# Optimization experiments

Hardware: AMD Instinct MI355X
Metric: run time of the kernel (lower is better)

Reference implementation:

```python
import jax, jax.numpy as jnp
import numpy as np

N_NODES, IN_DIM, HEADS, HEAD_DIM, OUT_DIM, N_GRAPHS, N_EDGES = 100000, 3, 4, 16, 2, 512, 3200000
NEG_SLOPE = 0.2  # PyG GATConv default negative_slope


def setup_inputs() -> dict:
    key = jax.random.key(0)
    ks = jax.random.split(key, 8)
    HC = HEADS * HEAD_DIM
    x = jax.random.normal(ks[0], (N_NODES, IN_DIM), dtype=jnp.float32)
    edge_index = jax.random.randint(ks[1], (2, N_EDGES), 0, N_NODES, dtype=jnp.int64)
    # sorted graph ids covering all N_GRAPHS segments (avoids empty-segment -inf in max pool)
    batch = (jnp.arange(N_NODES, dtype=jnp.int64) * N_GRAPHS) // N_NODES
    glorot = lambda k, shape, fan: jax.random.normal(k, shape, dtype=jnp.float32) * (1.0 / np.sqrt(fan))
    W = glorot(ks[2], (IN_DIM, HC), IN_DIM)          # GATConv lin weight
    att_src = glorot(ks[3], (HEADS, HEAD_DIM), HEAD_DIM)
    att_dst = glorot(ks[4], (HEADS, HEAD_DIM), HEAD_DIM)
    bias = jnp.zeros((HC,), dtype=jnp.float32)       # GATConv bias (concat=True)
    clf_W = glorot(ks[5], (HC, OUT_DIM), HC)
    clf_b = jnp.zeros((OUT_DIM,), dtype=jnp.float32)
    return {"feature_matrix": x, "edge_index": edge_index, "batch": batch,
            "W": W, "att_src": att_src, "att_dst": att_dst, "bias": bias,
            "clf_W": clf_W, "clf_b": clf_b}


def _gat_forward(x, edge_index, batch, W, att_src, att_dst, bias, clf_W, clf_b):
    N = x.shape[0]
    # PyG GATConv default: add self loops
    ar = jnp.arange(N, dtype=edge_index.dtype)
    ei = jnp.concatenate([edge_index, jnp.stack([ar, ar])], axis=1)
    src, dst = ei[0], ei[1]
    h = (x @ W).reshape(N, HEADS, HEAD_DIM)                     # [N,H,C]
    a_src = jnp.einsum('nhc,hc->nh', h, att_src)                # [N,H]
    a_dst = jnp.einsum('nhc,hc->nh', h, att_dst)
    e = jax.nn.leaky_relu(a_src[src] + a_dst[dst], NEG_SLOPE)   # [E,H]
    # softmax over edges grouped by destination node (every node has a self loop)
    m = jax.ops.segment_max(e, dst, num_segments=N)
    p = jnp.exp(e - m[dst])
    s = jax.ops.segment_sum(p, dst, num_segments=N)
    alpha = p / s[dst]                                          # [E,H]
    msg = h[src] * alpha[:, :, None]                            # [E,H,C]
    out = jax.ops.segment_sum(msg, dst, num_segments=N).reshape(N, HEADS * HEAD_DIM) + bias
    out = jax.nn.relu(out)
    pooled = jax.ops.segment_max(out, batch, num_segments=N_GRAPHS)  # [G,HC]
    return pooled @ clf_W + clf_b                               # [G,OUT]


def reference(feature_matrix, edge_index, batch, W, att_src, att_dst, bias, clf_W, clf_b):
    return _gat_forward(feature_matrix, edge_index, batch, W, att_src, att_dst, bias, clf_W, clf_b)
```

## Files before the change

### kernel.cpp

```cpp
#include <hip/hip_runtime.h>

#define NN 100000
#define NE 3200000
#define NE4 (NE / 4)
#define NG 512
#define OUTD 2
#define NEG_SLOPE 0.2f

#define CAP 81
#define BSZ 98
#define NSTR 1021
#define SCAP 3712
#define ADLS 5
#define EDGE_BLOCKS 256

__global__ __launch_bounds__(1024) void bin_kernel(const int* __restrict__ ei,
                                                   int* __restrict__ gcnt,
                                                   int* __restrict__ stream_) {
    __shared__ int cnt[NSTR];
    __shared__ int off[NSTR];
    int eb = blockIdx.x;
    int start = eb * 3125;
    int end = min(start + 3125, NE4);
    for (int i = threadIdx.x; i < NSTR; i += 1024) cnt[i] = 0;
    __syncthreads();
    int4 sv[4], dv[4];
    #pragma unroll
    for (int k = 0; k < 4; ++k) {
        int i4 = start + k * 1024 + threadIdx.x;
        if (i4 < end) {
            sv[k] = ((const int4*)ei)[i4];
            dv[k] = ((const int4*)(ei + NE))[i4];
            atomicAdd(&cnt[dv[k].x / BSZ], 1);
            atomicAdd(&cnt[dv[k].y / BSZ], 1);
            atomicAdd(&cnt[dv[k].z / BSZ], 1);
            atomicAdd(&cnt[dv[k].w / BSZ], 1);
        }
    }
    __syncthreads();
    for (int i = threadIdx.x; i < NSTR; i += 1024)
        off[i] = cnt[i] ? atomicAdd(&gcnt[i], cnt[i]) : 0;
    __syncthreads();
    #pragma unroll
    for (int k = 0; k < 4; ++k) {
        int i4 = start + k * 1024 + threadIdx.x;
        if (i4 < end) {
            int b, l, p;
            b = dv[k].x / BSZ; l = dv[k].x - b * BSZ; p = atomicAdd(&off[b], 1);
            stream_[(size_t)b * SCAP + p] = sv[k].x | (l << 17);
            b = dv[k].y / BSZ; l = dv[k].y - b * BSZ; p = atomicAdd(&off[b], 1);
            stream_[(size_t)b * SCAP + p] = sv[k].y | (l << 17);
            b = dv[k].z / BSZ; l = dv[k].z - b * BSZ; p = atomicAdd(&off[b], 1);
            stream_[(size_t)b * SCAP + p] = sv[k].z | (l << 17);
            b = dv[k].w / BSZ; l = dv[k].w - b * BSZ; p = atomicAdd(&off[b], 1);
            stream_[(size_t)b * SCAP + p] = sv[k].w | (l << 17);
        }
    }
}

__global__ __launch_bounds__(512) void gather_kernel(
        const int* __restrict__ gcnt, const int* __restrict__ stream_,
        const float* __restrict__ x, const float* __restrict__ W,
        const float* __restrict__ att_src, const float* __restrict__ att_dst,
        const float* __restrict__ bias, const int* __restrict__ batch,
        unsigned* __restrict__ pooled) {
    __shared__ int slots[BSZ * CAP];
    __shared__ int scnt[BSZ];
    __shared__ float xl[BSZ * 3];
    __shared__ float adl[BSZ * ADLS];
    __shared__ float Wl[192];
    __shared__ float wsS[12], wdS[12];
    __shared__ unsigned ploc[2 * 64];
    int b = blockIdx.x;
    int nbase = b * BSZ;
    if (nbase >= NN) return;
    int nloc = min(BSZ, NN - nbase);
    int tid = threadIdx.x;

    for (int i = tid; i < 192; i += 512) Wl[i] = W[i];
    for (int i = tid; i < nloc * 3; i += 512) xl[i] = x[nbase * 3 + i];
    if (tid < 24) {
        int t = tid % 12, j = t >> 2, h = t & 3;
        const float* att = (tid < 12) ? att_src : att_dst;
        float s = 0.f;
        #pragma unroll
        for (int c = 0; c < 16; ++c) s += W[j * 64 + h * 16 + c] * att[h * 16 + c];
        if (tid < 12) wsS[t] = s; else wdS[t] = s;
    }
    for (int i = tid; i < BSZ; i += 512) scnt[i] = 0;
    for (int i = tid; i < 128; i += 512) ploc[i] = 0;
    __syncthreads();
    for (int i = tid; i < nloc * 4; i += 512) {
        int l = i >> 2, h = i & 3;
        adl[l * ADLS + h] = xl[l * 3] * wdS[h] + xl[l * 3 + 1] * wdS[4 + h]
                          + xl[l * 3 + 2] * wdS[8 + h];
    }
    __syncthreads();

    int eg = gcnt[b];
    const int* st = stream_ + (size_t)b * SCAP;
    for (int i = tid; i < eg; i += 512) {
        int v = st[i];
        int s = v & 0x1FFFF;
        int l = v >> 17;
        int p = atomicAdd(&scnt[l], 1);
        if (p < CAP) slots[l * CAP + p] = s;
    }
    __syncthreads();

    int gbase = batch[nbase];
    int g = tid >> 2, head = tid & 3;
    if (g < nloc) {
        int n = nbase + g;
        float ws0 = wsS[head], ws1 = wsS[4 + head], ws2 = wsS[8 + head];
        float adh = adl[g * ADLS + head];
        float lx0 = xl[g * 3], lx1 = xl[g * 3 + 1], lx2 = xl[g * 3 + 2];

        float e = lx0 * ws0 + lx1 * ws1 + lx2 * ws2 + adh;
        e = e > 0.f ? e : NEG_SLOPE * e;
        float p = __expf(e);
        float sh = p, sx0 = p * lx0, sx1 = p * lx1, sx2 = p * lx2;

        int d = min(scnt[g], CAP);
        const int* row = &slots[g * CAP];
        int j = 0;
        for (; j + 3 < d; j += 4) {
            int sA = row[j], sB = row[j + 1], sC = row[j + 2], sD = row[j + 3];
            float xA0 = x[sA * 3], xA1 = x[sA * 3 + 1], xA2 = x[sA * 3 + 2];
            float xB0 = x[sB * 3], xB1 = x[sB * 3 + 1], xB2 = x[sB * 3 + 2];
            float xC0 = x[sC * 3], xC1 = x[sC * 3 + 1], xC2 = x[sC * 3 + 2];
            float xD0 = x[sD * 3], xD1 = x[sD * 3 + 1], xD2 = x[sD * 3 + 2];
            float eA = xA0 * ws0 + xA1 * ws1 + xA2 * ws2 + adh; eA = eA > 0.f ? eA : NEG_SLOPE * eA;
            float eB = xB0 * ws0 + xB1 * ws1 + xB2 * ws2 + adh; eB = eB > 0.f ? eB : NEG_SLOPE * eB;
            float eC = xC0 * ws0 + xC1 * ws1 + xC2 * ws2 + adh; eC = eC > 0.f ? eC : NEG_SLOPE * eC;
            float eD = xD0 * ws0 + xD1 * ws1 + xD2 * ws2 + adh; eD = eD > 0.f ? eD : NEG_SLOPE * eD;
            float pA = __expf(eA), pB = __expf(eB), pC = __expf(eC), pD = __expf(eD);
            sh  += (pA + pB) + (pC + pD);
            sx0 += pA * xA0 + pB * xB0 + pC * xC0 + pD * xD0;
            sx1 += pA * xA1 + pB * xB1 + pC * xC1 + pD * xD1;
            sx2 += pA * xA2 + pB * xB2 + pC * xC2 + pD * xD2;
        }
        for (; j < d; ++j) {
            int sA = row[j];
            float xA0 = x[sA * 3], xA1 = x[sA * 3 + 1], xA2 = x[sA * 3 + 2];
            float eA = xA0 * ws0 + xA1 * ws1 + xA2 * ws2 + adh; eA = eA > 0.f ? eA : NEG_SLOPE * eA;
            float pA = __expf(eA);
            sh += pA; sx0 += pA * xA0; sx1 += pA * xA1; sx2 += pA * xA2;
        }

        float inv = 1.f / sh;
        sx0 *= inv; sx1 *= inv; sx2 *= inv;
        int gl = batch[n] - gbase;
        unsigned* pb = ploc + gl * 64 + head * 16;
        const float* w0 = Wl + head * 16;
        const float* w1 = Wl + 64 + head * 16;
        const float* w2 = Wl + 128 + head * 16;
        const float* bv = bias + head * 16;
        #pragma unroll
        for (int k = 0; k < 16; ++k) {
            float vv = fmaxf(w0[k] * sx0 + w1[k] * sx1 + w2[k] * sx2 + bv[k], 0.f);
            atomicMax(&pb[k], __float_as_uint(vv));
        }
    }
    __syncthreads();
    for (int i = tid; i < 128; i += 512) {
        unsigned v = ploc[i];
        if (v) {
            int gid = gbase + (i >> 6);
            if (gid < NG) atomicMax(&pooled[gid * 64 + (i & 63)], v);
        }
    }
}

__global__ void clf_kernel(const unsigned* __restrict__ pooled, const float* __restrict__ clf_W,
                           const float* __restrict__ clf_b, float* __restrict__ out) {
    int i = blockIdx.x * blockDim.x + threadIdx.x;
    if (i >= NG * OUTD) return;
    int g = i >> 1, o = i & 1;
    float acc = clf_b[o];
    #pragma unroll
    for (int k = 0; k < 64; ++k)
        acc += __uint_as_float(pooled[g * 64 + k]) * clf_W[k * 2 + o];
    out[i] = acc;
}

extern "C" void kernel_launch(void* const* d_in, const int* in_sizes, int n_in,
                              void* d_out, int out_size, void* d_ws, size_t ws_size,
                              hipStream_t stream) {
    const float* x       = (const float*)d_in[0];
    const int*   ei      = (const int*)d_in[1];
    const int*   batch   = (const int*)d_in[2];
    const float* W       = (const float*)d_in[3];
    const float* att_src = (const float*)d_in[4];
    const float* att_dst = (const float*)d_in[5];
    const float* bias    = (const float*)d_in[6];
    const float* clf_W   = (const float*)d_in[7];
    const float* clf_b   = (const float*)d_in[8];
    float* out = (float*)d_out;

    int*      gcnt   = (int*)d_ws;
    unsigned* pooled = (unsigned*)(gcnt + NSTR);
    int*      stream_= (int*)(pooled + (size_t)NG * 64);

    hipMemsetAsync((void*)gcnt, 0, (NSTR + (size_t)NG * 64) * 4, stream);

    bin_kernel<<<EDGE_BLOCKS, 1024, 0, stream>>>(ei, gcnt, stream_);

    gather_kernel<<<NSTR, 512, 0, stream>>>(gcnt, stream_, x, W,
                                            att_src, att_dst, bias, batch, pooled);

    clf_kernel<<<(NG * OUTD + 255) / 256, 256, 0, stream>>>(pooled, clf_W, clf_b, out);
}
```

Baseline: 73.44 us.

## Split node edge list across four lanes, compute all heads per edge, shuffle-reduce

The gather loop used to have each of a node's four threads (one per head) walk the whole edge list and reload every neighbor's x. Now each of the four lanes takes a strided quarter of the edges and computes all four heads per edge. The per-head partial sums are then combined with xor shuffles, and each lane picks out its own head's totals. This cuts redundant global x loads by a factor of four, at the cost of four times the exp and FMA work per loaded edge, more registers, and a 16-value shuffle reduction.

```diff
diff --git a/kernel.cpp b/kernel.cpp
--- a/kernel.cpp
+++ b/kernel.cpp
@@ -19,8 +19,7 @@
                                                    int* __restrict__ stream_) {
     __shared__ int cnt[NSTR];
     __shared__ int off[NSTR];
-    int eb = blockIdx.x;
-    int start = eb * 3125;
+    int start = blockIdx.x * 3125;
     int end = min(start + 3125, NE4);
     for (int i = threadIdx.x; i < NSTR; i += 1024) cnt[i] = 0;
     __syncthreads();
@@ -109,57 +108,83 @@
     __syncthreads();
 
     int gbase = batch[nbase];
-    int g = tid >> 2, head = tid & 3;
+    int g = tid >> 2, k = tid & 3;
     if (g < nloc) {
         int n = nbase + g;
-        float ws0 = wsS[head], ws1 = wsS[4 + head], ws2 = wsS[8 + head];
-        float adh = adl[g * ADLS + head];
+        float wsr[12], adr[4];
+        #pragma unroll
+        for (int i = 0; i < 12; ++i) wsr[i] = wsS[i];
+        #pragma unroll
+        for (int h = 0; h < 4; ++h) adr[h] = adl[g * ADLS + h];
         float lx0 = xl[g * 3], lx1 = xl[g * 3 + 1], lx2 = xl[g * 3 + 2];
 
-        float e = lx0 * ws0 + lx1 * ws1 + lx2 * ws2 + adh;
-        e = e > 0.f ? e : NEG_SLOPE * e;
-        float p = __expf(e);
-        float sh = p, sx0 = p * lx0, sx1 = p * lx1, sx2 = p * lx2;
+        float acc[4][4];
+        #pragma unroll
+        for (int h = 0; h < 4; ++h)
+            #pragma unroll
+            for (int q = 0; q < 4; ++q) acc[h][q] = 0.f;
+
+#define EDGE_ACC(xx0, xx1, xx2)                                                 \
+        {                                                                       \
+            _Pragma("unroll")                                                   \
+            for (int h = 0; h < 4; ++h) {                                       \
+                float e = (xx0) * wsr[h] + (xx1) * wsr[4 + h]                   \
+                        + (xx2) * wsr[8 + h] + adr[h];                          \
+                e = e > 0.f ? e : NEG_SLOPE * e;                                \
+                float pp = __expf(e);                                           \
+                acc[h][0] += pp;                                                \
+                acc[h][1] += pp * (xx0);                                        \
+                acc[h][2] += pp * (xx1);                                        \
+                acc[h][3] += pp * (xx2);                                        \
+            }                                                                   \
+        }
+
+        if (k == 0) EDGE_ACC(lx0, lx1, lx2);
 
         int d = min(scnt[g], CAP);
         const int* row = &slots[g * CAP];
-        int j = 0;
-        for (; j + 3 < d; j += 4) {
-            int sA = row[j], sB = row[j + 1], sC = row[j + 2], sD = row[j + 3];
-            float xA0 = x[sA * 3], xA1 = x[sA * 3 + 1], xA2 = x[sA * 3 + 2];
-            float xB0 = x[sB * 3], xB1 = x[sB * 3 + 1], xB2 = x[sB * 3 + 2];
-            float xC0 = x[sC * 3], xC1 = x[sC * 3 + 1], xC2 = x[sC * 3 + 2];
-            float xD0 = x[sD * 3], xD1 = x[sD * 3 + 1], xD2 = x[sD * 3 + 2];
-            float eA = xA0 * ws0 + xA1 * ws1 + xA2 * ws2 + adh; eA = eA > 0.f ? eA : NEG_SLOPE * eA;
-            float eB = xB0 * ws0 + xB1 * ws1 + xB2 * ws2 + adh; eB = eB > 0.f ? eB : NEG_SLOPE * eB;
-            float eC = xC0 * ws0 + xC1 * ws1 + xC2 * ws2 + adh; eC = eC > 0.f ? eC : NEG_SLOPE * eC;
-            float eD = xD0 * ws0 + xD1 * ws1 + xD2 * ws2 + adh; eD = eD > 0.f ? eD : NEG_SLOPE * eD;
-            float pA = __expf(eA), pB = __expf(eB), pC = __expf(eC), pD = __expf(eD);
-            sh  += (pA + pB) + (pC + pD);
-            sx0 += pA * xA0 + pB * xB0 + pC * xC0 + pD * xD0;
-            sx1 += pA * xA1 + pB * xB1 + pC * xC1 + pD * xD1;
-            sx2 += pA * xA2 + pB * xB2 + pC * xC2 + pD * xD2;
-        }
-        for (; j < d; ++j) {
+        int j = k;
+        for (; j + 4 < d; j += 8) {
+            int sA = row[j], sB = row[j + 4];
+            float a0 = x[sA * 3], a1 = x[sA * 3 + 1], a2 = x[sA * 3 + 2];
+            float b0 = x[sB * 3], b1 = x[sB * 3 + 1], b2 = x[sB * 3 + 2];
+            EDGE_ACC(a0, a1, a2);
+            EDGE_ACC(b0, b1, b2);
+        }
+        if (j < d) {
             int sA = row[j];
-            float xA0 = x[sA * 3], xA1 = x[sA * 3 + 1], xA2 = x[sA * 3 + 2];
-            float eA = xA0 * ws0 + xA1 * ws1 + xA2 * ws2 + adh; eA = eA > 0.f ? eA : NEG_SLOPE * eA;
-            float pA = __expf(eA);
-            sh += pA; sx0 += pA * xA0; sx1 += pA * xA1; sx2 += pA * xA2;
-        }
+            float a0 = x[sA * 3], a1 = x[sA * 3 + 1], a2 = x[sA * 3 + 2];
+            EDGE_ACC(a0, a1, a2);
+        }
+#undef EDGE_ACC
+
+        #pragma unroll
+        for (int h = 0; h < 4; ++h)
+            #pragma unroll
+            for (int q = 0; q < 4; ++q) {
+                float v = acc[h][q];
+                v += __shfl_xor(v, 1);
+                v += __shfl_xor(v, 2);
+                acc[h][q] = v;
+            }
+
+        float sh  = k == 0 ? acc[0][0] : k == 1 ? acc[1][0] : k == 2 ? acc[2][0] : acc[3][0];
+        float sx0 = k == 0 ? acc[0][1] : k == 1 ? acc[1][1] : k == 2 ? acc[2][1] : acc[3][1];
+        float sx1 = k == 0 ? acc[0][2] : k == 1 ? acc[1][2] : k == 2 ? acc[2][2] : acc[3][2];
+        float sx2 = k == 0 ? acc[0][3] : k == 1 ? acc[1][3] : k == 2 ? acc[2][3] : acc[3][3];
 
         float inv = 1.f / sh;
         sx0 *= inv; sx1 *= inv; sx2 *= inv;
         int gl = batch[n] - gbase;
-        unsigned* pb = ploc + gl * 64 + head * 16;
-        const float* w0 = Wl + head * 16;
-        const float* w1 = Wl + 64 + head * 16;
-        const float* w2 = Wl + 128 + head * 16;
-        const float* bv = bias + head * 16;
-        #pragma unroll
-        for (int k = 0; k < 16; ++k) {
-            float vv = fmaxf(w0[k] * sx0 + w1[k] * sx1 + w2[k] * sx2 + bv[k], 0.f);
-            atomicMax(&pb[k], __float_as_uint(vv));
+        unsigned* pb = ploc + gl * 64 + k * 16;
+        const float* w0 = Wl + k * 16;
+        const float* w1 = Wl + 64 + k * 16;
+        const float* w2 = Wl + 128 + k * 16;
+        const float* bv = bias + k * 16;
+        #pragma unroll
+        for (int q = 0; q < 16; ++q) {
+            float vv = fmaxf(w0[q] * sx0 + w1[q] * sx1 + w2[q] * sx2 + bv[q], 0.f);
+            atomicMax(&pb[q], __float_as_uint(vv));
         }
     }
     __syncthreads();
```

After: 80.28 us. +9.3%, slower.
